# Kernel tuning notes

Measured on AMD Instinct MI355X. Metric: run time of the kernel, lower is better.

The kernel has to match this reference:

```python
import jax, jax.numpy as jnp
import numpy as np

N = 100000      # nodes
E = 1600000     # edges (avg degree 16)
F_N, F_E, H = 5, 3, 64
L = 3           # num GCN layers


def setup_inputs() -> dict:
    key = jax.random.key(0)
    ks = jax.random.split(key, 20)
    s = 0.05
    p = lambda k, shape: jax.random.normal(k, shape, jnp.float32) * s
    return {
        "x": jax.random.normal(ks[0], (N, F_N), jnp.float32),
        "edge_index": jax.random.randint(ks[1], (2, E), 0, N, dtype=jnp.int32),
        "edge_attr": jax.random.normal(ks[2], (E, F_E), jnp.float32),
        # node / edge encoders
        "Wn": p(ks[3], (F_N, H)), "bn": jnp.zeros((H,), jnp.float32),
        "We": p(ks[4], (F_E, H)), "be": jnp.zeros((H,), jnp.float32),
        # stacked GCNConv weights [L, H, H] and biases [L, H]
        "Wc": p(ks[5], (L, H, H)), "bc": jnp.zeros((L, H), jnp.float32),
        # demand forecast head
        "Wd1": p(ks[6], (H, H // 2)), "bd1": jnp.zeros((H // 2,), jnp.float32),
        "Wd2": p(ks[7], (H // 2, 1)), "bd2": jnp.zeros((1,), jnp.float32),
        # inventory optimizer head
        "Wi1": p(ks[8], (H, H // 2)), "bi1": jnp.zeros((H // 2,), jnp.float32),
        "Wi2": p(ks[9], (H // 2, 1)), "bi2": jnp.zeros((1,), jnp.float32),
    }


def reference(x, edge_index, edge_attr, Wn, bn, We, be, Wc, bc,
              Wd1, bd1, Wd2, bd2, Wi1, bi1, Wi2, bi2):
    src, dst = edge_index[0], edge_index[1]
    n = x.shape[0]

    h = jax.nn.relu(x @ Wn + bn)                      # [N, H]
    _ea = jax.nn.relu(edge_attr @ We + be)            # encoded edge feats (GCNConv ignores them)

    # GCN symmetric normalization with self-loops: deg[i] = in_degree(i) + 1
    ones_e = jnp.ones(src.shape[0], h.dtype)
    deg = jax.ops.segment_sum(ones_e, dst, num_segments=n) + 1.0
    dinv = jax.lax.rsqrt(deg)                         # [N]
    norm_e = dinv[src] * dinv[dst]                    # [E]
    norm_self = (dinv * dinv)[:, None]                # [N, 1]

    for l in range(Wc.shape[0]):
        hw = h @ Wc[l]                                # [N, H]
        msgs = norm_e[:, None] * hw[src]              # gather + scale, [E, H]
        agg = jax.ops.segment_sum(msgs, dst, num_segments=n) + norm_self * hw
        h = jax.nn.relu(agg + bc[l])

    demand = jax.nn.relu(h @ Wd1 + bd1) @ Wd2 + bd2   # [N, 1]
    inventory = jax.nn.relu(h @ Wi1 + bi1) @ Wi2 + bi2
    return demand, inventory
```

## Files before the change

kernel.cpp:

```cpp
#include <hip/hip_runtime.h>

#define H 64
#define FN 5
#define EPB 4096
#define BSHIFT 8
#define CAP2 4864

typedef _Float16 half4 __attribute__((ext_vector_type(4)));
typedef _Float16 half8 __attribute__((ext_vector_type(8)));
typedef float    float8v __attribute__((ext_vector_type(8)));

__global__ void k_bscatter2(const int* __restrict__ src, const int* __restrict__ dst,
                            int* __restrict__ lofs_g, int* __restrict__ bcounts,
                            int* __restrict__ binned, int nE, int nbB) {
    __shared__ int lh[512], lpos[512], lcur[512], tmp[256];
    __shared__ int stage[EPB];
    int t = threadIdx.x;
    int e0 = blockIdx.x * EPB;
    int es[16], ed[16];
    lh[t] = 0; lh[t + 256] = 0;
    __syncthreads();
#pragma unroll
    for (int i = 0; i < 16; ++i) {
        int e = e0 + i * 256 + t;
        bool v = e < nE;
        es[i] = v ? src[e] : 0;
        ed[i] = v ? dst[e] : -1;
        if (v) atomicAdd(&lh[ed[i] >> BSHIFT], 1);
    }
    __syncthreads();
    int a0 = lh[2 * t], a1 = lh[2 * t + 1];
    tmp[t] = a0 + a1;
    __syncthreads();
    for (int s = 1; s < 256; s <<= 1) {
        int a = (t >= s) ? tmp[t - s] : 0;
        __syncthreads();
        tmp[t] += a;
        __syncthreads();
    }
    int ex = tmp[t] - (a0 + a1);
    lpos[2 * t] = ex;
    lpos[2 * t + 1] = ex + a0;
    __syncthreads();
    lcur[t] = lpos[t]; lcur[t + 256] = lpos[t + 256];
    size_t row = (size_t)blockIdx.x * (nbB + 1);
    for (int b = t; b <= nbB; b += 256) lofs_g[row + b] = lpos[b];
    for (int b = t; b < nbB; b += 256) if (lh[b]) atomicAdd(&bcounts[b], lh[b]);
    __syncthreads();
#pragma unroll
    for (int i = 0; i < 16; ++i) {
        if (ed[i] >= 0) {
            int b = ed[i] >> BSHIFT;
            int p = atomicAdd(&lcur[b], 1);
            stage[p] = es[i] | ((ed[i] & 255) << 17);
        }
    }
    __syncthreads();
    int total = lpos[nbB];
    for (int j = t; j < total; j += 256) binned[e0 + j] = stage[j];
}

__global__ void k_bscan2(const int* __restrict__ bcounts, int* __restrict__ bbase, int nbB) {
    __shared__ int tmp[512];
    int t = threadIdx.x;
    int v = (t < nbB) ? bcounts[t] : 0;
    tmp[t] = v;
    __syncthreads();
    for (int s = 1; s < 512; s <<= 1) {
        int a = (t >= s) ? tmp[t - s] : 0;
        __syncthreads();
        tmp[t] += a;
        __syncthreads();
    }
    if (t < nbB) bbase[t + 1] = tmp[t];
    if (t == 0) bbase[0] = 0;
}

__global__ void k_bcsr2(const int* __restrict__ binned, const int* __restrict__ lofs_g,
                        const int* __restrict__ bbase, int* __restrict__ row_ptr,
                        int* __restrict__ csr_src, float* __restrict__ dinv,
                        int n, int nE, int nbE, int nbB) {
    __shared__ int len_s[512], start_s[512], roff[512], tmp[256];
    __shared__ int deg[256], st[256], cur[256];
    __shared__ int lbuf[CAP2];
    __shared__ int stage2[CAP2];
    int t = threadIdx.x;
    int B = blockIdx.x;
    int node0 = B << BSHIFT;
    int nn = min(256, n - node0);
    len_s[t] = 0; len_s[t + 256] = 0;
    __syncthreads();
    for (int sb = t; sb < nbE; sb += 256) {
        size_t row = (size_t)sb * (nbB + 1);
        int o0 = lofs_g[row + B], o1 = lofs_g[row + B + 1];
        len_s[sb] = o1 - o0;
        start_s[sb] = sb * EPB + o0;
    }
    __syncthreads();
    int a0 = len_s[2 * t], a1 = len_s[2 * t + 1];
    tmp[t] = a0 + a1;
    __syncthreads();
    for (int s = 1; s < 256; s <<= 1) {
        int a = (t >= s) ? tmp[t - s] : 0;
        __syncthreads();
        tmp[t] += a;
        __syncthreads();
    }
    int ex = tmp[t] - (a0 + a1);
    roff[2 * t] = ex;
    roff[2 * t + 1] = ex + a0;
    __syncthreads();
    int total = min(roff[511] + len_s[511], CAP2);
    for (int sb = t; sb < nbE; sb += 256) {
        int s0 = start_s[sb], ln = len_s[sb], d0 = roff[sb];
        for (int k = 0; k < ln; ++k) {
            int d = d0 + k;
            if (d < CAP2) lbuf[d] = binned[s0 + k];
        }
    }
    deg[t] = 0;
    __syncthreads();
    for (int i = t; i < total; i += 256) atomicAdd(&deg[(lbuf[i] >> 17) & 255], 1);
    __syncthreads();
    tmp[t] = deg[t];
    __syncthreads();
    for (int s = 1; s < 256; s <<= 1) {
        int a = (t >= s) ? tmp[t - s] : 0;
        __syncthreads();
        tmp[t] += a;
        __syncthreads();
    }
    st[t] = tmp[t] - deg[t];
    cur[t] = st[t];
    __syncthreads();
    int base = bbase[B];
    if (t < nn) {
        row_ptr[node0 + t] = base + st[t];
        dinv[node0 + t] = 1.0f / sqrtf((float)deg[t] + 1.0f);
    }
    if (B == 0 && t == 0) row_ptr[n] = nE;
    for (int i = t; i < total; i += 256) {
        int p0 = lbuf[i];
        int p = atomicAdd(&cur[(p0 >> 17) & 255], 1);
        int sv = p0 & 0x1FFFF;
        if (p < CAP2) stage2[p] = sv;
        else csr_src[base + p] = sv;
    }
    __syncthreads();
    for (int i = t; i < total; i += 256) csr_src[base + i] = stage2[i];
}

__global__ void k_enc(const float* __restrict__ x, const float* __restrict__ Wn,
                      const float* __restrict__ bn, const float* __restrict__ dinv,
                      _Float16* __restrict__ g0, int n) {
    int tid = blockIdx.x * 256 + threadIdx.x;
    int node = tid >> 6, ch = tid & 63;
    if (node >= n) return;
    float acc = bn[ch];
#pragma unroll
    for (int k = 0; k < FN; ++k)
        acc += x[(size_t)node * FN + k] * Wn[k * H + ch];
    g0[(size_t)node * H + ch] = (_Float16)(fmaxf(acc, 0.f) * dinv[node]);
}

__global__ void k_layer(const _Float16* __restrict__ gin, const int* __restrict__ csr_src,
                        const int* __restrict__ row_ptr, const float* __restrict__ dinv,
                        const float* __restrict__ W, const float* __restrict__ bias,
                        _Float16* __restrict__ gout, float* __restrict__ hout,
                        int n, int last) {
    __shared__ float As[64 * 68];
    __shared__ int rp_s[65];
    __shared__ float dv_s[64];
    int t = threadIdx.x;
    int wave = t >> 6, lane = t & 63;
    int base = blockIdx.x * 64;
    if (t < 65) rp_s[t] = row_ptr[min(base + t, n)];
    if (t >= 128 && t < 192) {
        int nd = base + (t - 128);
        dv_s[t - 128] = (nd < n) ? dinv[nd] : 0.f;
    }
    __syncthreads();

    int c8 = (lane >> 3) * 8;
    int slot = lane & 7;
    for (int it = 0; it < 8; ++it) {
        int rA = it * 8 + wave, rB = rA + 4;
        int nodeA = base + rA, nodeB = base + rB;
        float8v accA = 0.f, accB = 0.f;
        int iA = rp_s[rA], eA = rp_s[rA + 1];
        int iB = rp_s[rB], eB = rp_s[rB + 1];
        while (iA + 8 <= eA && iB + 8 <= eB) {
            int xA = csr_src[iA + slot];
            int xB = csr_src[iB + slot];
            half8 vA = *(const half8*)(gin + (size_t)xA * H + c8);
            half8 vB = *(const half8*)(gin + (size_t)xB * H + c8);
#pragma unroll
            for (int k = 0; k < 8; ++k) { accA[k] += (float)vA[k]; accB[k] += (float)vB[k]; }
            iA += 8; iB += 8;
        }
        while (iA + 8 <= eA) {
            int xA = csr_src[iA + slot];
            half8 vA = *(const half8*)(gin + (size_t)xA * H + c8);
#pragma unroll
            for (int k = 0; k < 8; ++k) accA[k] += (float)vA[k];
            iA += 8;
        }
        while (iB + 8 <= eB) {
            int xB = csr_src[iB + slot];
            half8 vB = *(const half8*)(gin + (size_t)xB * H + c8);
#pragma unroll
            for (int k = 0; k < 8; ++k) accB[k] += (float)vB[k];
            iB += 8;
        }
        if (iA + slot < eA) {
            int xA = csr_src[iA + slot];
            half8 vA = *(const half8*)(gin + (size_t)xA * H + c8);
#pragma unroll
            for (int k = 0; k < 8; ++k) accA[k] += (float)vA[k];
        }
        if (iB + slot < eB) {
            int xB = csr_src[iB + slot];
            half8 vB = *(const half8*)(gin + (size_t)xB * H + c8);
#pragma unroll
            for (int k = 0; k < 8; ++k) accB[k] += (float)vB[k];
        }
#pragma unroll
        for (int m = 1; m <= 4; m <<= 1) {
#pragma unroll
            for (int k = 0; k < 8; ++k) {
                accA[k] += __shfl_xor(accA[k], m, 64);
                accB[k] += __shfl_xor(accB[k], m, 64);
            }
        }
        if (slot == 0) {
            float oA[8], oB[8];
            if (nodeA < n) {
                half8 sA = *(const half8*)(gin + (size_t)nodeA * H + c8);
                float dA = dv_s[rA];
#pragma unroll
                for (int k = 0; k < 8; ++k) oA[k] = (accA[k] + (float)sA[k]) * dA;
            } else {
#pragma unroll
                for (int k = 0; k < 8; ++k) oA[k] = 0.f;
            }
            if (nodeB < n) {
                half8 sB = *(const half8*)(gin + (size_t)nodeB * H + c8);
                float dB = dv_s[rB];
#pragma unroll
                for (int k = 0; k < 8; ++k) oB[k] = (accB[k] + (float)sB[k]) * dB;
            } else {
#pragma unroll
                for (int k = 0; k < 8; ++k) oB[k] = 0.f;
            }
            *(float4*)&As[rA * 68 + c8]     = make_float4(oA[0], oA[1], oA[2], oA[3]);
            *(float4*)&As[rA * 68 + c8 + 4] = make_float4(oA[4], oA[5], oA[6], oA[7]);
            *(float4*)&As[rB * 68 + c8]     = make_float4(oB[0], oB[1], oB[2], oB[3]);
            *(float4*)&As[rB * 68 + c8 + 4] = make_float4(oB[4], oB[5], oB[6], oB[7]);
        }
    }
    __syncthreads();

    int tx = t & 15, ty = t >> 4;
    int c0 = tx * 4;
    const float* a0 = As + (ty * 4 + 0) * 68;
    const float* a1 = As + (ty * 4 + 1) * 68;
    const float* a2 = As + (ty * 4 + 2) * 68;
    const float* a3 = As + (ty * 4 + 3) * 68;
    float4 acc0 = make_float4(0.f, 0.f, 0.f, 0.f);
    float4 acc1 = acc0, acc2 = acc0, acc3 = acc0;
#pragma unroll 16
    for (int k = 0; k < H; ++k) {
        float4 w = *(const float4*)(W + k * H + c0);
        float v0 = a0[k], v1 = a1[k], v2 = a2[k], v3 = a3[k];
        acc0.x += v0 * w.x; acc0.y += v0 * w.y; acc0.z += v0 * w.z; acc0.w += v0 * w.w;
        acc1.x += v1 * w.x; acc1.y += v1 * w.y; acc1.z += v1 * w.z; acc1.w += v1 * w.w;
        acc2.x += v2 * w.x; acc2.y += v2 * w.y; acc2.z += v2 * w.z; acc2.w += v2 * w.w;
        acc3.x += v3 * w.x; acc3.y += v3 * w.y; acc3.z += v3 * w.z; acc3.w += v3 * w.w;
    }
    float4 b = *(const float4*)(bias + c0);
    float4 accs[4] = {acc0, acc1, acc2, acc3};
#pragma unroll
    for (int rr = 0; rr < 4; ++rr) {
        int r = ty * 4 + rr;
        int row = base + r;
        if (row < n) {
            float4 o;
            o.x = fmaxf(accs[rr].x + b.x, 0.f);
            o.y = fmaxf(accs[rr].y + b.y, 0.f);
            o.z = fmaxf(accs[rr].z + b.z, 0.f);
            o.w = fmaxf(accs[rr].w + b.w, 0.f);
            if (last) {
                *(float4*)(hout + (size_t)row * H + c0) = o;
            } else {
                float d = dv_s[r];
                half4 hh;
                hh.x = (_Float16)(o.x * d);
                hh.y = (_Float16)(o.y * d);
                hh.z = (_Float16)(o.z * d);
                hh.w = (_Float16)(o.w * d);
                *(half4*)(gout + (size_t)row * H + c0) = hh;
            }
        }
    }
}

__global__ void k_heads(const float* __restrict__ h,
                        const float* __restrict__ Wd1, const float* __restrict__ bd1,
                        const float* __restrict__ Wd2, const float* __restrict__ bd2,
                        const float* __restrict__ Wi1, const float* __restrict__ bi1,
                        const float* __restrict__ Wi2, const float* __restrict__ bi2,
                        float* __restrict__ out, int n) {
    __shared__ float hs[64 * 65];
    int lane = threadIdx.x;
    int base = blockIdx.x * 64;
    for (int r = 0; r < 64; ++r) {
        int row = base + r;
        hs[r * 65 + lane] = (row < n) ? h[(size_t)row * H + lane] : 0.f;
    }
    __syncthreads();

    float accd[32], acci[32];
#pragma unroll
    for (int j = 0; j < 32; ++j) { accd[j] = bd1[j]; acci[j] = bi1[j]; }
    for (int k = 0; k < H; ++k) {
        float hk = hs[lane * 65 + k];
#pragma unroll
        for (int j = 0; j < 32; ++j) {
            accd[j] += hk * Wd1[k * 32 + j];
            acci[j] += hk * Wi1[k * 32 + j];
        }
    }
    float demand = bd2[0], inventory = bi2[0];
#pragma unroll
    for (int j = 0; j < 32; ++j) {
        demand    += fmaxf(accd[j], 0.f) * Wd2[j];
        inventory += fmaxf(acci[j], 0.f) * Wi2[j];
    }
    int node = base + lane;
    if (node < n) {
        out[node] = demand;
        out[n + node] = inventory;
    }
}

extern "C" void kernel_launch(void* const* d_in, const int* in_sizes, int n_in,
                              void* d_out, int out_size, void* d_ws, size_t ws_size,
                              hipStream_t stream) {
    const float* x   = (const float*)d_in[0];
    const int*   ei  = (const int*)  d_in[1];
    const float* Wn  = (const float*)d_in[3];
    const float* bn  = (const float*)d_in[4];
    const float* Wc  = (const float*)d_in[7];
    const float* bc  = (const float*)d_in[8];
    const float* Wd1 = (const float*)d_in[9];
    const float* bd1 = (const float*)d_in[10];
    const float* Wd2 = (const float*)d_in[11];
    const float* bd2 = (const float*)d_in[12];
    const float* Wi1 = (const float*)d_in[13];
    const float* bi1 = (const float*)d_in[14];
    const float* Wi2 = (const float*)d_in[15];
    const float* bi2 = (const float*)d_in[16];

    const int n  = in_sizes[0] / FN;
    const int nE = in_sizes[1] / 2;
    const int* src = ei;
    const int* dst = ei + nE;

    const int nbE = (nE + EPB - 1) / EPB;
    const int nbB = (n + 255) >> BSHIFT;
    const int nbL = (n + 63) / 64;

    char* w = (char*)d_ws;
    int* binned    = (int*)w;   w += (size_t)nbE * EPB * 4;
    int* csr_src   = (int*)w;   w += (size_t)nE * 4;
    int* row_ptr   = (int*)w;   w += (size_t)(n + 4) * 4;
    float* dinv    = (float*)w; w += (size_t)n * 4;
    int* lofs      = (int*)w;   w += (size_t)nbE * (nbB + 1) * 4;
    int* bcounts   = (int*)w;   w += 512 * 4;
    int* bbase     = (int*)w;   w += 516 * 4;
    float* hbuf    = (float*)w; w += (size_t)n * H * 4;
    _Float16* gA   = (_Float16*)w; w += (size_t)n * H * 2;
    _Float16* gB   = (_Float16*)w; w += (size_t)n * H * 2;

    hipMemsetAsync(bcounts, 0, 512 * 4, stream);

    k_bscatter2<<<nbE, 256, 0, stream>>>(src, dst, lofs, bcounts, binned, nE, nbB);
    k_bscan2   <<<1,   512, 0, stream>>>(bcounts, bbase, nbB);
    k_bcsr2    <<<nbB, 256, 0, stream>>>(binned, lofs, bbase, row_ptr, csr_src,
                                         dinv, n, nE, nbE, nbB);

    k_enc<<<((size_t)n * 64 + 255) / 256, 256, 0, stream>>>(x, Wn, bn, dinv, gA, n);

    k_layer<<<nbL, 256, 0, stream>>>(gA, csr_src, row_ptr, dinv, Wc,
                                     bc, gB, hbuf, n, 0);
    k_layer<<<nbL, 256, 0, stream>>>(gB, csr_src, row_ptr, dinv, Wc + (size_t)H * H,
                                     bc + H, gA, hbuf, n, 0);
    k_layer<<<nbL, 256, 0, stream>>>(gA, csr_src, row_ptr, dinv, Wc + (size_t)2 * H * H,
                                     bc + 2 * H, gB, hbuf, n, 1);

    k_heads<<<(n + 63) / 64, 64, 0, stream>>>(hbuf, Wd1, bd1, Wd2, bd2,
                                              Wi1, bi1, Wi2, bi2, (float*)d_out, n);
}
```

Baseline: 387.7 us.

## Fold bucket scan into CSR build, binary-search copy, shrink layer tiles

Removes the separate single-block scan kernel by having each CSR-build block reduce the bucket counts before it to get its own base offset. Replaces the per-run serial copy loop with a flat per-element loop that binary-searches the run offsets, which spreads the copy evenly across threads. Shrinks the GCN layer tile from 64 to 16 nodes per block, giving more blocks and smaller shared memory for better load balance and occupancy. In exchange, each thread in the layer GEMM gets less register reuse of W, and every CSR block repeats a partial reduction over the bucket counts.

```diff
diff --git a/kernel.cpp b/kernel.cpp
--- a/kernel.cpp
+++ b/kernel.cpp
@@ -60,44 +60,40 @@
     for (int j = t; j < total; j += 256) binned[e0 + j] = stage[j];
 }
 
-__global__ void k_bscan2(const int* __restrict__ bcounts, int* __restrict__ bbase, int nbB) {
-    __shared__ int tmp[512];
-    int t = threadIdx.x;
-    int v = (t < nbB) ? bcounts[t] : 0;
-    tmp[t] = v;
-    __syncthreads();
-    for (int s = 1; s < 512; s <<= 1) {
-        int a = (t >= s) ? tmp[t - s] : 0;
-        __syncthreads();
-        tmp[t] += a;
-        __syncthreads();
-    }
-    if (t < nbB) bbase[t + 1] = tmp[t];
-    if (t == 0) bbase[0] = 0;
-}
-
 __global__ void k_bcsr2(const int* __restrict__ binned, const int* __restrict__ lofs_g,
-                        const int* __restrict__ bbase, int* __restrict__ row_ptr,
+                        const int* __restrict__ bcounts, int* __restrict__ row_ptr,
                         int* __restrict__ csr_src, float* __restrict__ dinv,
                         int n, int nE, int nbE, int nbB) {
-    __shared__ int len_s[512], start_s[512], roff[512], tmp[256];
+    __shared__ int runlen[512], runstart[512], roff[512], tmp[256];
     __shared__ int deg[256], st[256], cur[256];
+    __shared__ int sh_base, sh_total;
     __shared__ int lbuf[CAP2];
     __shared__ int stage2[CAP2];
     int t = threadIdx.x;
     int B = blockIdx.x;
     int node0 = B << BSHIFT;
     int nn = min(256, n - node0);
-    len_s[t] = 0; len_s[t + 256] = 0;
+
+    int myb = 0;
+    for (int b = t; b < B; b += 256) myb += bcounts[b];
+    tmp[t] = myb;
+    __syncthreads();
+    for (int s = 128; s > 0; s >>= 1) {
+        if (t < s) tmp[t] += tmp[t + s];
+        __syncthreads();
+    }
+    if (t == 0) sh_base = tmp[0];
+
+    runlen[t] = 0; runlen[t + 256] = 0;
     __syncthreads();
     for (int sb = t; sb < nbE; sb += 256) {
         size_t row = (size_t)sb * (nbB + 1);
         int o0 = lofs_g[row + B], o1 = lofs_g[row + B + 1];
-        len_s[sb] = o1 - o0;
-        start_s[sb] = sb * EPB + o0;
-    }
-    __syncthreads();
-    int a0 = len_s[2 * t], a1 = len_s[2 * t + 1];
+        runlen[sb] = o1 - o0;
+        runstart[sb] = sb * EPB + o0;
+    }
+    __syncthreads();
+    int a0 = runlen[2 * t], a1 = runlen[2 * t + 1];
     tmp[t] = a0 + a1;
     __syncthreads();
     for (int s = 1; s < 256; s <<= 1) {
@@ -109,14 +105,17 @@
     int ex = tmp[t] - (a0 + a1);
     roff[2 * t] = ex;
     roff[2 * t + 1] = ex + a0;
-    __syncthreads();
-    int total = min(roff[511] + len_s[511], CAP2);
-    for (int sb = t; sb < nbE; sb += 256) {
-        int s0 = start_s[sb], ln = len_s[sb], d0 = roff[sb];
-        for (int k = 0; k < ln; ++k) {
-            int d = d0 + k;
-            if (d < CAP2) lbuf[d] = binned[s0 + k];
-        }
+    if (t == 255) sh_total = tmp[255];
+    __syncthreads();
+    int total = min(sh_total, CAP2);
+
+    for (int j = t; j < total; j += 256) {
+        int lo = 0, hi = nbE - 1;
+        while (lo < hi) {
+            int mid = (lo + hi + 1) >> 1;
+            if (roff[mid] <= j) lo = mid; else hi = mid - 1;
+        }
+        lbuf[j] = binned[runstart[lo] + (j - roff[lo])];
     }
     deg[t] = 0;
     __syncthreads();
@@ -133,7 +132,7 @@
     st[t] = tmp[t] - deg[t];
     cur[t] = st[t];
     __syncthreads();
-    int base = bbase[B];
+    int base = sh_base;
     if (t < nn) {
         row_ptr[node0 + t] = base + st[t];
         dinv[node0 + t] = 1.0f / sqrtf((float)deg[t] + 1.0f);
@@ -168,22 +167,23 @@
                         const float* __restrict__ W, const float* __restrict__ bias,
                         _Float16* __restrict__ gout, float* __restrict__ hout,
                         int n, int last) {
-    __shared__ float As[64 * 68];
-    __shared__ int rp_s[65];
-    __shared__ float dv_s[64];
+    __shared__ float As[16 * 68];
+    __shared__ int rp_s[17];
+    __shared__ float dv_s[16];
     int t = threadIdx.x;
     int wave = t >> 6, lane = t & 63;
-    int base = blockIdx.x * 64;
-    if (t < 65) rp_s[t] = row_ptr[min(base + t, n)];
-    if (t >= 128 && t < 192) {
-        int nd = base + (t - 128);
-        dv_s[t - 128] = (nd < n) ? dinv[nd] : 0.f;
+    int base = blockIdx.x * 16;
+    if (t < 17) rp_s[t] = row_ptr[min(base + t, n)];
+    if (t >= 64 && t < 80) {
+        int nd = base + (t - 64);
+        dv_s[t - 64] = (nd < n) ? dinv[nd] : 0.f;
     }
     __syncthreads();
 
     int c8 = (lane >> 3) * 8;
     int slot = lane & 7;
-    for (int it = 0; it < 8; ++it) {
+#pragma unroll
+    for (int it = 0; it < 2; ++it) {
         int rA = it * 8 + wave, rB = rA + 4;
         int nodeA = base + rA, nodeB = base + rB;
         float8v accA = 0.f, accB = 0.f;
@@ -262,44 +262,32 @@
 
     int tx = t & 15, ty = t >> 4;
     int c0 = tx * 4;
-    const float* a0 = As + (ty * 4 + 0) * 68;
-    const float* a1 = As + (ty * 4 + 1) * 68;
-    const float* a2 = As + (ty * 4 + 2) * 68;
-    const float* a3 = As + (ty * 4 + 3) * 68;
-    float4 acc0 = make_float4(0.f, 0.f, 0.f, 0.f);
-    float4 acc1 = acc0, acc2 = acc0, acc3 = acc0;
+    const float* A0 = As + ty * 68;
+    float4 acc = make_float4(0.f, 0.f, 0.f, 0.f);
 #pragma unroll 16
     for (int k = 0; k < H; ++k) {
         float4 w = *(const float4*)(W + k * H + c0);
-        float v0 = a0[k], v1 = a1[k], v2 = a2[k], v3 = a3[k];
-        acc0.x += v0 * w.x; acc0.y += v0 * w.y; acc0.z += v0 * w.z; acc0.w += v0 * w.w;
-        acc1.x += v1 * w.x; acc1.y += v1 * w.y; acc1.z += v1 * w.z; acc1.w += v1 * w.w;
-        acc2.x += v2 * w.x; acc2.y += v2 * w.y; acc2.z += v2 * w.z; acc2.w += v2 * w.w;
-        acc3.x += v3 * w.x; acc3.y += v3 * w.y; acc3.z += v3 * w.z; acc3.w += v3 * w.w;
+        float v0 = A0[k];
+        acc.x += v0 * w.x; acc.y += v0 * w.y; acc.z += v0 * w.z; acc.w += v0 * w.w;
     }
     float4 b = *(const float4*)(bias + c0);
-    float4 accs[4] = {acc0, acc1, acc2, acc3};
-#pragma unroll
-    for (int rr = 0; rr < 4; ++rr) {
-        int r = ty * 4 + rr;
-        int row = base + r;
-        if (row < n) {
-            float4 o;
-            o.x = fmaxf(accs[rr].x + b.x, 0.f);
-            o.y = fmaxf(accs[rr].y + b.y, 0.f);
-            o.z = fmaxf(accs[rr].z + b.z, 0.f);
-            o.w = fmaxf(accs[rr].w + b.w, 0.f);
-            if (last) {
-                *(float4*)(hout + (size_t)row * H + c0) = o;
-            } else {
-                float d = dv_s[r];
-                half4 hh;
-                hh.x = (_Float16)(o.x * d);
-                hh.y = (_Float16)(o.y * d);
-                hh.z = (_Float16)(o.z * d);
-                hh.w = (_Float16)(o.w * d);
-                *(half4*)(gout + (size_t)row * H + c0) = hh;
-            }
+    int row = base + ty;
+    if (row < n) {
+        float4 o;
+        o.x = fmaxf(acc.x + b.x, 0.f);
+        o.y = fmaxf(acc.y + b.y, 0.f);
+        o.z = fmaxf(acc.z + b.z, 0.f);
+        o.w = fmaxf(acc.w + b.w, 0.f);
+        if (last) {
+            *(float4*)(hout + (size_t)row * H + c0) = o;
+        } else {
+            float d = dv_s[ty];
+            half4 hh;
+            hh.x = (_Float16)(o.x * d);
+            hh.y = (_Float16)(o.y * d);
+            hh.z = (_Float16)(o.z * d);
+            hh.w = (_Float16)(o.w * d);
+            *(half4*)(gout + (size_t)row * H + c0) = hh;
         }
     }
 }
@@ -368,7 +356,7 @@
 
     const int nbE = (nE + EPB - 1) / EPB;
     const int nbB = (n + 255) >> BSHIFT;
-    const int nbL = (n + 63) / 64;
+    const int nbL = (n + 15) / 16;
 
     char* w = (char*)d_ws;
     int* binned    = (int*)w;   w += (size_t)nbE * EPB * 4;
@@ -377,7 +365,6 @@
     float* dinv    = (float*)w; w += (size_t)n * 4;
     int* lofs      = (int*)w;   w += (size_t)nbE * (nbB + 1) * 4;
     int* bcounts   = (int*)w;   w += 512 * 4;
-    int* bbase     = (int*)w;   w += 516 * 4;
     float* hbuf    = (float*)w; w += (size_t)n * H * 4;
     _Float16* gA   = (_Float16*)w; w += (size_t)n * H * 2;
     _Float16* gB   = (_Float16*)w; w += (size_t)n * H * 2;
@@ -385,8 +372,7 @@
     hipMemsetAsync(bcounts, 0, 512 * 4, stream);
 
     k_bscatter2<<<nbE, 256, 0, stream>>>(src, dst, lofs, bcounts, binned, nE, nbB);
-    k_bscan2   <<<1,   512, 0, stream>>>(bcounts, bbase, nbB);
-    k_bcsr2    <<<nbB, 256, 0, stream>>>(binned, lofs, bbase, row_ptr, csr_src,
+    k_bcsr2    <<<nbB, 256, 0, stream>>>(binned, lofs, bcounts, row_ptr, csr_src,
                                          dinv, n, nE, nbE, nbB);
 
     k_enc<<<((size_t)n * 64 + 255) / 256, 256, 0, stream>>>(x, Wn, bn, dinv, gA, n);
```

Result: slower. 459.0 us (+18.4%).
